# Optimization experiments

Measured on AMD Instinct MI355X. Metric: run time of the kernel, lower is better.

The kernel has to match this reference:

```python
import jax, jax.numpy as jnp
import numpy as np

LN_EPS = 1e-5

def setup_inputs() -> dict:
    key = jax.random.key(0)
    ks = jax.random.split(key, 10)
    B, L, D2 = 64, 512, 16  # batch, max_len_text, 2*n_degree
    V, D, C = 8000, 256, 4  # n_word, d_model, n_category
    E = (V - 1) * V + 1      # edge-weight table size
    x = jax.random.randint(ks[0], (B, L), 0, V, dtype=jnp.int32)
    nb_x = jax.random.randint(ks[1], (B, L, D2), 0, V, dtype=jnp.int32)
    w_edge = jax.random.randint(ks[2], (B, L, D2), 0, E, dtype=jnp.int32)
    emb_weight = jax.random.normal(ks[3], (V, D), jnp.float32) * 0.02
    emb_weight = emb_weight.at[0].set(0.0)  # padding_idx=0
    w_edge_table = jax.random.normal(ks[4], (E, 1), jnp.float32) * 0.02
    w_edge_table = w_edge_table.at[0].set(0.0)
    eta_table = jax.random.normal(ks[5], (V, 1), jnp.float32) * 0.02
    eta_table = eta_table.at[0].set(0.0)
    ln_gamma = jnp.ones((D,), jnp.float32)
    ln_beta = jnp.zeros((D,), jnp.float32)
    fc_w = jax.random.normal(ks[6], (D, C), jnp.float32) * 0.02
    fc_b = jnp.zeros((C,), jnp.float32)
    return {"x": x, "nb_x": nb_x, "w_edge": w_edge,
            "emb_weight": emb_weight, "w_edge_table": w_edge_table,
            "eta_table": eta_table, "ln_gamma": ln_gamma, "ln_beta": ln_beta,
            "fc_w": fc_w, "fc_b": fc_b}

def _layernorm(h, gamma, beta):
    mu = jnp.mean(h, axis=-1, keepdims=True)
    var = jnp.mean(jnp.square(h - mu), axis=-1, keepdims=True)
    return (h - mu) * jax.lax.rsqrt(var + LN_EPS) * gamma + beta

def reference(x, nb_x, w_edge, emb_weight, w_edge_table, eta_table,
              ln_gamma, ln_beta, fc_w, fc_b):
    # idx_nodes: (B, L, 2*deg + 1) -- neighbors then self
    idx_nodes = jnp.concatenate([nb_x, x[..., None]], axis=-1)
    emb_nodes = emb_weight[idx_nodes]                  # (B, L, 2d+1, D)
    emb_nodes = _layernorm(emb_nodes, ln_gamma, ln_beta)
    we = w_edge_table[w_edge]                          # (B, L, 2d, 1)
    msg_nb = jnp.max(we * emb_nodes[:, :, :-1, :], axis=2)  # (B, L, D)
    eta = eta_table[x]                                 # (B, L, 1)
    h_node = (1.0 - eta) * msg_nb + eta * emb_nodes[:, :, -1, :]
    scores = h_node.sum(axis=1) @ fc_w + fc_b          # (B, C)
    return scores
```

## Files before the change

kernel.cpp:

```cpp
#include <hip/hip_runtime.h>
#include <math.h>

#define DV   256
#define BB   64
#define LL   512
#define DEG2 16
#define VV   8000
#define CC   4
#define LPW  4
#define NW   4
#define NLC  32
#define LN_EPS 1e-5f

typedef _Float16 half4 __attribute__((ext_vector_type(4)));
typedef _Float16 half8 __attribute__((ext_vector_type(8)));
typedef float    f32x4 __attribute__((ext_vector_type(4)));
typedef int      i32x4 __attribute__((ext_vector_type(4)));

__device__ __forceinline__ int rl(int v, int lane) {
    return __builtin_amdgcn_readlane(v, lane);
}
__device__ __forceinline__ float rlf(float v, int lane) {
    return __int_as_float(__builtin_amdgcn_readlane(__float_as_int(v), lane));
}
__device__ __forceinline__ half8 swap32h8(half8 v) {
    i32x4 i = __builtin_bit_cast(i32x4, v);
    i32x4 s;
    #pragma unroll
    for (int k = 0; k < 4; ++k) s[k] = __shfl_xor(i[k], 32);
    return __builtin_bit_cast(half8, s);
}

__global__ void __launch_bounds__(64) ln_rows_kernel(
    const float* __restrict__ emb, const float* __restrict__ gamma,
    const float* __restrict__ beta, half4* __restrict__ out)
{
    const int row = blockIdx.x;
    const int ln  = threadIdx.x;

    const f32x4 v = ((const f32x4*)(emb + row * DV))[ln];

    float s = v[0] + v[1] + v[2] + v[3];
    #pragma unroll
    for (int off = 32; off > 0; off >>= 1) s += __shfl_xor(s, off);
    const float mu = s * (1.0f / DV);

    f32x4 c;
    #pragma unroll
    for (int k = 0; k < 4; ++k) c[k] = v[k] - mu;

    float q = c[0]*c[0] + c[1]*c[1] + c[2]*c[2] + c[3]*c[3];
    #pragma unroll
    for (int off = 32; off > 0; off >>= 1) q += __shfl_xor(q, off);
    const float rs = rsqrtf(q * (1.0f / DV) + LN_EPS);

    const f32x4 g  = ((const f32x4*)gamma)[ln];
    const f32x4 bt = ((const f32x4*)beta)[ln];

    half4 h;
    #pragma unroll
    for (int k = 0; k < 4; ++k) h[k] = (_Float16)(c[k] * rs * g[k] + bt[k]);
    out[row * 64 + ln] = h;
}

__global__ void __launch_bounds__(256) gnn_kernel(
    const int*   __restrict__ nb_x,
    const int*   __restrict__ w_edge,
    const float* __restrict__ we_table,
    const int*   __restrict__ x,
    const float* __restrict__ eta_table,
    const half8* __restrict__ norm_emb,
    float*       __restrict__ h_part)
{
    const int b   = blockIdx.x;
    const int lc  = blockIdx.y;
    const int tid = threadIdx.x;
    const int w   = tid >> 6;
    const int ln  = tid & 63;
    const int c   = ln & 31;
    const int hi8 = (ln >> 5) << 3;

    const int l0   = lc * 16 + w * LPW;
    const int base = b * LL + l0;

    const int   nbv = __builtin_nontemporal_load(nb_x   + base * DEG2 + ln);
    const int   eiv = __builtin_nontemporal_load(w_edge + base * DEG2 + ln);
    const float wev = __builtin_nontemporal_load(we_table + eiv);

    int xv = 0; float etv = 0.0f;
    if (ln < LPW) { xv = x[base + ln]; etv = eta_table[xv]; }

    float acc[8] = {0,0,0,0,0,0,0,0};

    #pragma unroll
    for (int li = 0; li < LPW; ++li) {
        half8 m;
        #pragma unroll
        for (int k = 0; k < 8; ++k) m[k] = (_Float16)(-65504.0f);

        #pragma unroll
        for (int k = 0; k < 8; ++k) {
            const int   jsrc = li * DEG2 + k + hi8;
            const int   idx  = __shfl(nbv, jsrc);
            const float wj   = __shfl(wev, jsrc);
            half8 w8;
            #pragma unroll
            for (int q = 0; q < 8; ++q) w8[q] = (_Float16)wj;
            const half8 e = norm_emb[idx * 32 + c];
            m = __builtin_elementwise_max(m, w8 * e);
        }
        m = __builtin_elementwise_max(m, swap32h8(m));

        const int   sidx = rl(xv, li);
        const float eta  = rlf(etv, li);
        const half8 se   = norm_emb[sidx * 32 + c];
        const float om   = 1.0f - eta;
        #pragma unroll
        for (int k = 0; k < 8; ++k)
            acc[k] += om * (float)m[k] + eta * (float)se[k];
    }

    __shared__ float s_acc[NW][DV];
    if (ln < 32) {
        f32x4 a0 = {acc[0], acc[1], acc[2], acc[3]};
        f32x4 a1 = {acc[4], acc[5], acc[6], acc[7]};
        ((f32x4*)&s_acc[w][c * 8])[0] = a0;
        ((f32x4*)&s_acc[w][c * 8])[1] = a1;
    }
    __syncthreads();
    if (w == 0) {
        f32x4 r0 = ((f32x4*)s_acc[0])[ln];
        f32x4 r1 = ((f32x4*)s_acc[1])[ln];
        f32x4 r2 = ((f32x4*)s_acc[2])[ln];
        f32x4 r3 = ((f32x4*)s_acc[3])[ln];
        f32x4 r;
        #pragma unroll
        for (int k = 0; k < 4; ++k) r[k] = r0[k] + r1[k] + r2[k] + r3[k];
        __builtin_nontemporal_store(r, (f32x4*)(h_part + (size_t)(b * NLC + lc) * DV) + ln);
    }
}

__global__ void __launch_bounds__(256) fc_kernel(
    const float* __restrict__ h_part,
    const float* __restrict__ fc_w,
    const float* __restrict__ fc_b,
    float*       __restrict__ out)
{
    const int b  = blockIdx.x;
    const int d  = threadIdx.x;
    const int w  = d >> 6;
    const int ln = d & 63;

    float h = 0.0f;
    #pragma unroll 8
    for (int lc = 0; lc < NLC; ++lc)
        h += h_part[(size_t)(b * NLC + lc) * DV + d];

    float p[CC];
    #pragma unroll
    for (int c = 0; c < CC; ++c) p[c] = h * fc_w[d * CC + c];

    #pragma unroll
    for (int c = 0; c < CC; ++c)
        #pragma unroll
        for (int off = 32; off > 0; off >>= 1) p[c] += __shfl_xor(p[c], off);

    __shared__ float s_red[NW][CC];
    if (ln == 0) {
        #pragma unroll
        for (int c = 0; c < CC; ++c) s_red[w][c] = p[c];
    }
    __syncthreads();
    if (d < CC)
        out[b * CC + d] = s_red[0][d] + s_red[1][d] + s_red[2][d] + s_red[3][d] + fc_b[d];
}

extern "C" void kernel_launch(void* const* d_in, const int* in_sizes, int n_in,
                              void* d_out, int out_size, void* d_ws, size_t ws_size,
                              hipStream_t stream) {
    const int*   x        = (const int*)  d_in[0];
    const int*   nb_x     = (const int*)  d_in[1];
    const int*   w_edge   = (const int*)  d_in[2];
    const float* emb_w    = (const float*)d_in[3];
    const float* we_table = (const float*)d_in[4];
    const float* eta_tab  = (const float*)d_in[5];
    const float* ln_gamma = (const float*)d_in[6];
    const float* ln_beta  = (const float*)d_in[7];
    const float* fc_w     = (const float*)d_in[8];
    const float* fc_b     = (const float*)d_in[9];
    float* out = (float*)d_out;

    char* ws = (char*)d_ws;
    half4* norm_emb = (half4*)(ws);
    float* h_part   = (float*)(ws + 4096000);

    ln_rows_kernel<<<VV, 64, 0, stream>>>(emb_w, ln_gamma, ln_beta, norm_emb);

    dim3 grid2(BB, NLC);
    gnn_kernel<<<grid2, 256, 0, stream>>>(nb_x, w_edge, we_table, x, eta_tab,
                                          (const half8*)norm_emb, h_part);

    fc_kernel<<<BB, 256, 0, stream>>>(h_part, fc_w, fc_b, out);
}
```

Before: 43.90 us.

## Split embedding table into XCD-affine halves and pre-gather edge weights

Measured after the change: 43.11 us. About the same (-1.8%).

```diff
diff --git a/kernel.cpp b/kernel.cpp
--- a/kernel.cpp
+++ b/kernel.cpp
@@ -10,34 +10,36 @@
 #define LPW  4
 #define NW   4
 #define NLC  32
+#define NSL  2
+#define NE   (BB*LL*DEG2)
 #define LN_EPS 1e-5f
 
 typedef _Float16 half4 __attribute__((ext_vector_type(4)));
 typedef _Float16 half8 __attribute__((ext_vector_type(8)));
+typedef float    f32x2 __attribute__((ext_vector_type(2)));
 typedef float    f32x4 __attribute__((ext_vector_type(4)));
 typedef int      i32x4 __attribute__((ext_vector_type(4)));
 
-__device__ __forceinline__ int rl(int v, int lane) {
-    return __builtin_amdgcn_readlane(v, lane);
-}
-__device__ __forceinline__ float rlf(float v, int lane) {
-    return __int_as_float(__builtin_amdgcn_readlane(__float_as_int(v), lane));
-}
-__device__ __forceinline__ half8 swap32h8(half8 v) {
+__device__ __forceinline__ half8 sxor_h8(half8 v, int mask) {
     i32x4 i = __builtin_bit_cast(i32x4, v);
     i32x4 s;
     #pragma unroll
-    for (int k = 0; k < 4; ++k) s[k] = __shfl_xor(i[k], 32);
+    for (int k = 0; k < 4; ++k) s[k] = __shfl_xor(i[k], mask);
     return __builtin_bit_cast(half8, s);
 }
 
 __global__ void __launch_bounds__(64) ln_rows_kernel(
     const float* __restrict__ emb, const float* __restrict__ gamma,
-    const float* __restrict__ beta, half4* __restrict__ out)
+    const float* __restrict__ beta,
+    const int* __restrict__ w_edge, const float* __restrict__ we_table,
+    half4* __restrict__ out, float* __restrict__ we_flat)
 {
     const int row = blockIdx.x;
     const int ln  = threadIdx.x;
 
+    for (int g = blockIdx.x * 64 + ln; g < NE; g += VV * 64)
+        we_flat[g] = we_table[w_edge[g]];
+
     const f32x4 v = ((const f32x4*)(emb + row * DV))[ln];
 
     float s = v[0] + v[1] + v[2] + v[3];
@@ -60,36 +62,49 @@
     half4 h;
     #pragma unroll
     for (int k = 0; k < 4; ++k) h[k] = (_Float16)(c[k] * rs * g[k] + bt[k]);
-    out[row * 64 + ln] = h;
+
+    const int sl = ln >> 5;
+    const int cc = ln & 31;
+    ((half4*)out)[((size_t)sl * VV + row) * 32 + cc] = h;
 }
 
 __global__ void __launch_bounds__(256) gnn_kernel(
     const int*   __restrict__ nb_x,
-    const int*   __restrict__ w_edge,
-    const float* __restrict__ we_table,
     const int*   __restrict__ x,
+    const float* __restrict__ we_flat,
     const float* __restrict__ eta_table,
     const half8* __restrict__ norm_emb,
     float*       __restrict__ h_part)
 {
-    const int b   = blockIdx.x;
-    const int lc  = blockIdx.y;
+    const int blk = blockIdx.x;
+    const int xcd = blk & 7;
+    const int u   = blk >> 3;
+    const int sl  = xcd >> 2;
+    const int qq  = (xcd & 3) + (u << 2);
+    const int b   = qq >> 5;
+    const int lc  = qq & 31;
+
     const int tid = threadIdx.x;
     const int w   = tid >> 6;
     const int ln  = tid & 63;
-    const int c   = ln & 31;
-    const int hi8 = (ln >> 5) << 3;
+    const int q   = ln >> 4;
+    const int c8  = ln & 15;
 
     const int l0   = lc * 16 + w * LPW;
     const int base = b * LL + l0;
-
-    const int   nbv = __builtin_nontemporal_load(nb_x   + base * DEG2 + ln);
-    const int   eiv = __builtin_nontemporal_load(w_edge + base * DEG2 + ln);
-    const float wev = __builtin_nontemporal_load(we_table + eiv);
+    const size_t sRow = (size_t)sl * VV;
+
+    const int   nbv = __builtin_nontemporal_load(nb_x    + base * DEG2 + ln);
+    const float wev = __builtin_nontemporal_load(we_flat + base * DEG2 + ln);
 
     int xv = 0; float etv = 0.0f;
     if (ln < LPW) { xv = x[base + ln]; etv = eta_table[xv]; }
 
+    const int   srow = __shfl(xv, q);
+    const half8 se   = norm_emb[(sRow + srow) * 16 + c8];
+    const float eta  = __shfl(etv, q);
+    const float om   = 1.0f - eta;
+
     float acc[8] = {0,0,0,0,0,0,0,0};
 
     #pragma unroll
@@ -99,44 +114,47 @@
         for (int k = 0; k < 8; ++k) m[k] = (_Float16)(-65504.0f);
 
         #pragma unroll
-        for (int k = 0; k < 8; ++k) {
-            const int   jsrc = li * DEG2 + k + hi8;
+        for (int k4 = 0; k4 < 4; ++k4) {
+            const int   jsrc = li * DEG2 + k4 * 4 + q;
             const int   idx  = __shfl(nbv, jsrc);
             const float wj   = __shfl(wev, jsrc);
             half8 w8;
             #pragma unroll
-            for (int q = 0; q < 8; ++q) w8[q] = (_Float16)wj;
-            const half8 e = norm_emb[idx * 32 + c];
+            for (int t = 0; t < 8; ++t) w8[t] = (_Float16)wj;
+            const half8 e = norm_emb[(sRow + idx) * 16 + c8];
             m = __builtin_elementwise_max(m, w8 * e);
         }
-        m = __builtin_elementwise_max(m, swap32h8(m));
-
-        const int   sidx = rl(xv, li);
-        const float eta  = rlf(etv, li);
-        const half8 se   = norm_emb[sidx * 32 + c];
-        const float om   = 1.0f - eta;
-        #pragma unroll
-        for (int k = 0; k < 8; ++k)
-            acc[k] += om * (float)m[k] + eta * (float)se[k];
-    }
-
-    __shared__ float s_acc[NW][DV];
-    if (ln < 32) {
+        m = __builtin_elementwise_max(m, sxor_h8(m, 16));
+        m = __builtin_elementwise_max(m, sxor_h8(m, 32));
+
+        if (q == li) {
+            #pragma unroll
+            for (int k = 0; k < 8; ++k)
+                acc[k] += om * (float)m[k] + eta * (float)se[k];
+        }
+    }
+
+    #pragma unroll
+    for (int k = 0; k < 8; ++k) {
+        acc[k] += __shfl_xor(acc[k], 16);
+        acc[k] += __shfl_xor(acc[k], 32);
+    }
+
+    __shared__ float s_acc[NW][DV / NSL];
+    if (ln < 16) {
         f32x4 a0 = {acc[0], acc[1], acc[2], acc[3]};
         f32x4 a1 = {acc[4], acc[5], acc[6], acc[7]};
-        ((f32x4*)&s_acc[w][c * 8])[0] = a0;
-        ((f32x4*)&s_acc[w][c * 8])[1] = a1;
+        ((f32x4*)&s_acc[w][c8 * 8])[0] = a0;
+        ((f32x4*)&s_acc[w][c8 * 8])[1] = a1;
     }
     __syncthreads();
     if (w == 0) {
-        f32x4 r0 = ((f32x4*)s_acc[0])[ln];
-        f32x4 r1 = ((f32x4*)s_acc[1])[ln];
-        f32x4 r2 = ((f32x4*)s_acc[2])[ln];
-        f32x4 r3 = ((f32x4*)s_acc[3])[ln];
-        f32x4 r;
-        #pragma unroll
-        for (int k = 0; k < 4; ++k) r[k] = r0[k] + r1[k] + r2[k] + r3[k];
-        __builtin_nontemporal_store(r, (f32x4*)(h_part + (size_t)(b * NLC + lc) * DV) + ln);
+        const int d2 = ln * 2;
+        f32x2 r;
+        r[0] = s_acc[0][d2]     + s_acc[1][d2]     + s_acc[2][d2]     + s_acc[3][d2];
+        r[1] = s_acc[0][d2 + 1] + s_acc[1][d2 + 1] + s_acc[2][d2 + 1] + s_acc[3][d2 + 1];
+        __builtin_nontemporal_store(r,
+            (f32x2*)(h_part + (size_t)(b * NLC + lc) * DV + sl * (DV / NSL)) + ln);
     }
 }
 
@@ -192,13 +210,14 @@
 
     char* ws = (char*)d_ws;
     half4* norm_emb = (half4*)(ws);
-    float* h_part   = (float*)(ws + 4096000);
-
-    ln_rows_kernel<<<VV, 64, 0, stream>>>(emb_w, ln_gamma, ln_beta, norm_emb);
-
-    dim3 grid2(BB, NLC);
-    gnn_kernel<<<grid2, 256, 0, stream>>>(nb_x, w_edge, we_table, x, eta_tab,
-                                          (const half8*)norm_emb, h_part);
+    float* we_flat  = (float*)(ws + 4096000);
+    float* h_part   = (float*)(ws + 4096000 + 2097152);
+
+    ln_rows_kernel<<<VV, 64, 0, stream>>>(emb_w, ln_gamma, ln_beta,
+                                          w_edge, we_table, norm_emb, we_flat);
+
+    gnn_kernel<<<BB * NLC * NSL, 256, 0, stream>>>(
+        nb_x, x, we_flat, eta_tab, (const half8*)norm_emb, h_part);
 
     fc_kernel<<<BB, 256, 0, stream>>>(h_part, fc_w, fc_b, out);
 }
```
